# Optimization experiments

Measured on AMD Instinct MI355X. Metric: run time of the kernel, lower is better.

## Reference

```python
import jax, jax.numpy as jnp
import numpy as np

N = 8192
IN_F = 512
OUT_F = 512
ALPHA = 0.2          # LeakyReLU negative slope
NEG_INF = -9e15      # matches masked_fill value in the torch source


def setup_inputs() -> dict:
    key = jax.random.key(0)
    k1, k2, k3, k4, k5 = jax.random.split(key, 5)
    x = jax.random.normal(k1, (N, IN_F), dtype=jnp.float32)
    adj = jax.random.randint(k2, (N, N), 0, 2, dtype=jnp.int32)
    # nn.Linear(in, out, bias=False) stores weight as [out, in]
    W = jax.random.normal(k3, (OUT_F, IN_F), dtype=jnp.float32) / np.sqrt(IN_F)
    # nn.Linear(2*out, 1) weight [1, 2*out] split into the two halves that
    # act on h_i (a1) and h_j (a2): a([h_i, h_j]) = a1.h_i + a2.h_j
    a1 = jax.random.normal(k4, (OUT_F,), dtype=jnp.float32) / np.sqrt(2 * OUT_F)
    a2 = jax.random.normal(k5, (OUT_F,), dtype=jnp.float32) / np.sqrt(2 * OUT_F)
    return {"x": x, "adj": adj, "W": W, "a1": a1, "a2": a2}


def reference(x, adj, W, a1, a2):
    # h = W(x)                                  [N, OUT_F]
    h = x @ W.T
    # e[i, j] = leakyrelu(a . [h_i, h_j]) = leakyrelu(a1.h_i + a2.h_j)
    # (identical math to the N^2 concat in the source, without materializing it)
    src = h @ a1                                # [N]
    dst = h @ a2                                # [N]
    e = jax.nn.leaky_relu(src[:, None] + dst[None, :], negative_slope=ALPHA)
    e = jnp.where(adj == 0, jnp.float32(NEG_INF), e)
    attention = jax.nn.softmax(e, axis=1)       # [N, N]
    # dropout prob is 0.0 (eval-equivalent), so it is the identity
    h_prime = attention @ h                     # [N, OUT_F]
    return h_prime
```

## Files before the change

kernel.cpp:

```cpp
#include <hip/hip_runtime.h>
#include <hip/hip_bf16.h>
#include <stdint.h>

#define NN 8192
#define KF 512
#define ALPHA 0.2f
#define NT 64

typedef __bf16 bf16;
typedef __bf16 bf16x4 __attribute__((ext_vector_type(4)));
typedef __bf16 bf16x8 __attribute__((ext_vector_type(8)));
typedef float  f32x4  __attribute__((ext_vector_type(4)));
typedef float  f32x16 __attribute__((ext_vector_type(16)));

static constexpr size_t OFF_HQ  = 0;
static constexpr size_t OFF_XB  = (size_t)8 << 20;
static constexpr size_t OFF_WB  = (size_t)16 << 20;
static constexpr size_t OFF_SRC = OFF_WB + ((size_t)512 << 10);
static constexpr size_t OFF_DST = OFF_SRC + (size_t)NN * 4;
static constexpr size_t OFF_PRT = (size_t)17 << 20;
static constexpr size_t OFF_PDN = OFF_PRT + ((size_t)32 << 20);


__global__ void k_cvt(const float* __restrict__ x, const float* __restrict__ W,
                      bf16* __restrict__ xb, bf16* __restrict__ wb) {
    const int XQ = (NN * KF) / 4;
    const int TQ = XQ + (KF * KF) / 4;
    for (int i = blockIdx.x * blockDim.x + threadIdx.x; i < TQ;
         i += gridDim.x * blockDim.x) {
        const float4* s;
        bf16* d;
        int o;
        if (i < XQ) { s = (const float4*)x; d = xb; o = i; }
        else        { s = (const float4*)W; d = wb; o = i - XQ; }
        float4 v = s[o];
        bf16x4 b;
        b[0] = (bf16)v.x; b[1] = (bf16)v.y; b[2] = (bf16)v.z; b[3] = (bf16)v.w;
        *(bf16x4*)(d + (size_t)o * 4) = b;
    }
}

__global__ __launch_bounds__(256) void k_gemm(
    const bf16* __restrict__ xb, const bf16* __restrict__ wb,
    bf16* __restrict__ hQ, float* __restrict__ srcv, float* __restrict__ dstv,
    const float* __restrict__ a1, const float* __restrict__ a2) {
    const int tid = threadIdx.x;
    const int wv = tid >> 6;
    const int l = tid & 63;
    const int task = blockIdx.x * 4 + wv;
    const int rg = task >> 3, cc = task & 7;
    const int i0 = rg * 16, c0 = cc * 64;
    const int lr16 = l & 15, lk = l >> 4;

    f32x4 acc0 = {0.f,0.f,0.f,0.f}, acc1 = acc0, acc2 = acc0, acc3 = acc0;

    const bf16* ap  = xb + (size_t)(i0 + lr16) * KF + lk * 8;
    const bf16* bp0 = wb + (size_t)(c0 +  0 + lr16) * KF + lk * 8;
    const bf16* bp1 = wb + (size_t)(c0 + 16 + lr16) * KF + lk * 8;
    const bf16* bp2 = wb + (size_t)(c0 + 32 + lr16) * KF + lk * 8;
    const bf16* bp3 = wb + (size_t)(c0 + 48 + lr16) * KF + lk * 8;

#pragma unroll 4
    for (int k = 0; k < 16; ++k) {
        bf16x8 a  = *(const bf16x8*)(ap  + k * 32);
        bf16x8 b0 = *(const bf16x8*)(bp0 + k * 32);
        bf16x8 b1 = *(const bf16x8*)(bp1 + k * 32);
        bf16x8 b2 = *(const bf16x8*)(bp2 + k * 32);
        bf16x8 b3 = *(const bf16x8*)(bp3 + k * 32);
        acc0 = __builtin_amdgcn_mfma_f32_16x16x32_bf16(a, b0, acc0, 0, 0, 0);
        acc1 = __builtin_amdgcn_mfma_f32_16x16x32_bf16(a, b1, acc1, 0, 0, 0);
        acc2 = __builtin_amdgcn_mfma_f32_16x16x32_bf16(a, b2, acc2, 0, 0, 0);
        acc3 = __builtin_amdgcn_mfma_f32_16x16x32_bf16(a, b3, acc3, 0, 0, 0);
    }

    const int ib = i0 + lk * 4;
    const int jt = ib >> 6, kq = (ib >> 3) & 7, jr0 = ib & 7;
    float sr[4] = {0.f,0.f,0.f,0.f}, dr[4] = {0.f,0.f,0.f,0.f};
#pragma unroll
    for (int ct = 0; ct < 4; ++ct) {
        const f32x4 av = (ct == 0) ? acc0 : (ct == 1) ? acc1 : (ct == 2) ? acc2 : acc3;
        const int c = c0 + ct * 16 + lr16;
        const float A1 = a1[c], A2 = a2[c];
        bf16x4 hb;
#pragma unroll
        for (int r = 0; r < 4; ++r) {
            float h = av[r];
            sr[r] += h * A1;
            dr[r] += h * A2;
            hb[r] = (bf16)h;
        }
        *(bf16x4*)(hQ + ((size_t)(jt * 8 + kq) * 512 + c) * 8 + jr0) = hb;
    }
#pragma unroll
    for (int r = 0; r < 4; ++r) {
        float s = sr[r], d = dr[r];
        s += __shfl_xor(s, 1, 64); d += __shfl_xor(d, 1, 64);
        s += __shfl_xor(s, 2, 64); d += __shfl_xor(d, 2, 64);
        s += __shfl_xor(s, 4, 64); d += __shfl_xor(d, 4, 64);
        s += __shfl_xor(s, 8, 64); d += __shfl_xor(d, 8, 64);
        if (lr16 == 0) {
            atomicAdd(srcv + ib + r, s);
            atomicAdd(dstv + ib + r, d);
        }
    }
}

__global__ __launch_bounds__(512, 2) void k_attn(
    const int* __restrict__ adj, const bf16* __restrict__ hQ,
    const float* __restrict__ srcv, const float* __restrict__ dstv,
    float* __restrict__ part, float* __restrict__ pden) {
    __shared__ bf16 pl[64][72];
    __shared__ float dls[64];

    const int tid = threadIdx.x;
    const int l = tid & 63;
    const int wv = tid >> 6;
    const int bid = blockIdx.x;
    const int xg = bid & 7, qg = bid >> 3;
    const int js = xg >> 2;
    const int rt = qg * 4 + (xg & 3);
    const int i0 = rt * 64;
    const int jbase = js * 4096;

    const int pr = tid >> 3;
    const int pj = (tid & 7) * 8;
    const float si = srcv[i0 + pr];

    if (tid < 64) dls[tid] = 0.f;
    __syncthreads();

    const int lhi = l >> 5;
    const int l31 = l & 31;
    const int cA = wv * 64 + l31;

    const int*   adjp = adj  + (size_t)(i0 + pr) * NN + jbase + pj;
    const float* dstp = dstv + jbase + pj;
    const bf16*  hqb  = hQ + (size_t)cA * 8;
    const size_t tq0  = (size_t)js * 512;

    f32x16 acc00 = {0.f}, acc01 = {0.f}, acc10 = {0.f}, acc11 = {0.f};

    int4   adjA0 = *(const int4*)(adjp);
    int4   adjA1 = *(const int4*)(adjp + 4);
    float4 dstA0 = *(const float4*)(dstp);
    float4 dstA1 = *(const float4*)(dstp + 4);
    bf16x8 bfA[8], bfB[8];
#pragma unroll
    for (int k2 = 0; k2 < 4; ++k2) {
        bfA[k2 * 2]     = *(const bf16x8*)(hqb + (tq0 + k2 * 2 + lhi) * 4096);
        bfA[k2 * 2 + 1] = *(const bf16x8*)(hqb + (tq0 + k2 * 2 + lhi) * 4096 + 256);
    }
    int4 adjB0, adjB1;
    float4 dstB0, dstB1;

#define BODY(T, BFC, BFN, AJC0, AJC1, AJN0, AJN1, DSC0, DSC1, DSN0, DSN1)          \
    {                                                                              \
        const int t_ = (T);                                                        \
        if (t_ < NT - 1) {   \
            AJN0 = *(const int4*)(adjp + (t_ + 1) * 64);                           \
            AJN1 = *(const int4*)(adjp + (t_ + 1) * 64 + 4);                       \
        }                                                                          \
        {                                                                          \
            float w0,w1,w2,w3,w4,w5,w6,w7, e;                                      \
            e = si + DSC0.x; e = e > 0.f ? e : ALPHA * e; w0 = AJC0.x ? __expf(e) : 0.f; \
            e = si + DSC0.y; e = e > 0.f ? e : ALPHA * e; w1 = AJC0.y ? __expf(e) : 0.f; \
            e = si + DSC0.z; e = e > 0.f ? e : ALPHA * e; w2 = AJC0.z ? __expf(e) : 0.f; \
            e = si + DSC0.w; e = e > 0.f ? e : ALPHA * e; w3 = AJC0.w ? __expf(e) : 0.f; \
            e = si + DSC1.x; e = e > 0.f ? e : ALPHA * e; w4 = AJC1.x ? __expf(e) : 0.f; \
            e = si + DSC1.y; e = e > 0.f ? e : ALPHA * e; w5 = AJC1.y ? __expf(e) : 0.f; \
            e = si + DSC1.z; e = e > 0.f ? e : ALPHA * e; w6 = AJC1.z ? __expf(e) : 0.f; \
            e = si + DSC1.w; e = e > 0.f ? e : ALPHA * e; w7 = AJC1.w ? __expf(e) : 0.f; \
            bf16x8 pb;                                                             \
            pb[0]=(bf16)w0; pb[1]=(bf16)w1; pb[2]=(bf16)w2; pb[3]=(bf16)w3;        \
            pb[4]=(bf16)w4; pb[5]=(bf16)w5; pb[6]=(bf16)w6; pb[7]=(bf16)w7;        \
            *(bf16x8*)(&pl[pr][pj]) = pb;                                          \
            float dsum = w0+w1+w2+w3+w4+w5+w6+w7;                                  \
            dsum += __shfl_xor(dsum, 1, 64);                                       \
            dsum += __shfl_xor(dsum, 2, 64);                                       \
            dsum += __shfl_xor(dsum, 4, 64);                                       \
            if ((tid & 7) == 0) dls[pr] += dsum;                                   \
        }                                                                          \
        asm volatile("s_waitcnt lgkmcnt(0)" ::: "memory");                         \
        __builtin_amdgcn_s_barrier();                                              \
        if (t_ < NT - 1) {       \
            const size_t tqn = tq0 + (size_t)(t_ + 1) * 8;                         \
            _Pragma("unroll")                                                      \
            for (int k2 = 0; k2 < 4; ++k2) {                                       \
                BFN[k2 * 2]     = *(const bf16x8*)(hqb + (tqn + k2 * 2 + lhi) * 4096);       \
                BFN[k2 * 2 + 1] = *(const bf16x8*)(hqb + (tqn + k2 * 2 + lhi) * 4096 + 256); \
            }                                                                      \
            DSN0 = *(const float4*)(dstp + (t_ + 1) * 64);                         \
            DSN1 = *(const float4*)(dstp + (t_ + 1) * 64 + 4);                     \
        }                                                                          \
        _Pragma("unroll")                                                          \
        for (int k = 0; k < 4; ++k) {                                              \
            const int ko = k * 16 + lhi * 8;                                       \
            bf16x8 a0  = *(const bf16x8*)(&pl[l31][ko]);                           \
            bf16x8 a1f = *(const bf16x8*)(&pl[32 + l31][ko]);                      \
            acc00 = __builtin_amdgcn_mfma_f32_32x32x16_bf16(a0,  BFC[k*2],   acc00, 0,0,0); \
            acc01 = __builtin_amdgcn_mfma_f32_32x32x16_bf16(a0,  BFC[k*2+1], acc01, 0,0,0); \
            acc10 = __builtin_amdgcn_mfma_f32_32x32x16_bf16(a1f, BFC[k*2],   acc10, 0,0,0); \
            acc11 = __builtin_amdgcn_mfma_f32_32x32x16_bf16(a1f, BFC[k*2+1], acc11, 0,0,0); \
        }                                                                          \
        asm volatile("s_waitcnt lgkmcnt(0)" ::: "memory");                         \
        __builtin_amdgcn_s_barrier();                                              \
    }

    for (int tt = 0; tt < NT / 2; ++tt) {
        BODY(2 * tt,     bfA, bfB, adjA0, adjA1, adjB0, adjB1, dstA0, dstA1, dstB0, dstB1)
        BODY(2 * tt + 1, bfB, bfA, adjB0, adjB1, adjA0, adjA1, dstB0, dstB1, dstA0, dstA1)
    }
#undef BODY

    float* pp = part + (size_t)js * NN * KF;
#pragma unroll
    for (int g = 0; g < 16; ++g) {
        const int row = (g & 3) + 8 * (g >> 2) + 4 * lhi;
        pp[(size_t)(i0 + row) * KF + cA]           = acc00[g];
        pp[(size_t)(i0 + row) * KF + cA + 32]      = acc01[g];
        pp[(size_t)(i0 + 32 + row) * KF + cA]      = acc10[g];
        pp[(size_t)(i0 + 32 + row) * KF + cA + 32] = acc11[g];
    }
    if (tid < 64) pden[(size_t)js * NN + i0 + tid] = dls[tid];
}

__global__ void k_red(const float* __restrict__ part, const float* __restrict__ pden,
                      float* __restrict__ out) {
    int idx = blockIdx.x * blockDim.x + threadIdx.x;
    const float4 p0 = *(const float4*)(part + (size_t)idx * 4);
    const float4 p1 = *(const float4*)(part + (size_t)NN * KF + (size_t)idx * 4);
    int i = idx >> 7;
    float inv = 1.f / (pden[i] + pden[NN + i]);
    float4 o;
    o.x = (p0.x + p1.x) * inv;
    o.y = (p0.y + p1.y) * inv;
    o.z = (p0.z + p1.z) * inv;
    o.w = (p0.w + p1.w) * inv;
    *(float4*)(out + (size_t)idx * 4) = o;
}

extern "C" void kernel_launch(void* const* d_in, const int* in_sizes, int n_in,
                              void* d_out, int out_size, void* d_ws, size_t ws_size,
                              hipStream_t stream) {
    (void)in_sizes; (void)n_in; (void)out_size; (void)ws_size;
    const float* x  = (const float*)d_in[0];
    const int* adj  = (const int*)d_in[1];
    const float* W  = (const float*)d_in[2];
    const float* a1 = (const float*)d_in[3];
    const float* a2 = (const float*)d_in[4];
    float* out = (float*)d_out;
    char* ws = (char*)d_ws;

    bf16* hQ  = (bf16*)(ws + OFF_HQ);
    bf16* xb  = (bf16*)(ws + OFF_XB);
    bf16* wb  = (bf16*)(ws + OFF_WB);
    float* sv = (float*)(ws + OFF_SRC);
    float* dv = (float*)(ws + OFF_DST);
    float* part = (float*)(ws + OFF_PRT);
    float* pden = (float*)(ws + OFF_PDN);

    hipMemsetAsync(sv, 0, (size_t)2 * NN * sizeof(float), stream);
    k_cvt<<<2048, 256, 0, stream>>>(x, W, xb, wb);
    k_gemm<<<1024, 256, 0, stream>>>(xb, wb, hQ, sv, dv, a1, a2);
    k_attn<<<256, 512, 0, stream>>>(adj, hQ, sv, dv, part, pden);
    k_red<<<4096, 256, 0, stream>>>(part, pden, out);
}
```

Measured before the change: 507.2 us.

## Double-buffer attention LDS tile to drop one barrier per step

Double-buffers the shared P tile so each iteration needs a single barrier instead of two. The per-row denominator is kept in a register and reduced once at the end rather than updated in LDS every step. The loop is rolled back from the manual two-step unrolled macro, and next-tile prefetches are issued before the barrier. The launch-bounds occupancy hint of 2 is removed, which may raise register use and lower occupancy.

```diff
diff --git a/kernel.cpp b/kernel.cpp
--- a/kernel.cpp
+++ b/kernel.cpp
@@ -5,7 +5,7 @@
 #define NN 8192
 #define KF 512
 #define ALPHA 0.2f
-#define NT 64
+#define NTT 64
 
 typedef __bf16 bf16;
 typedef __bf16 bf16x4 __attribute__((ext_vector_type(4)));
@@ -105,12 +105,11 @@
     }
 }
 
-__global__ __launch_bounds__(512, 2) void k_attn(
+__global__ __launch_bounds__(512) void k_attn(
     const int* __restrict__ adj, const bf16* __restrict__ hQ,
     const float* __restrict__ srcv, const float* __restrict__ dstv,
     float* __restrict__ part, float* __restrict__ pden) {
-    __shared__ bf16 pl[64][72];
-    __shared__ float dls[64];
+    __shared__ bf16 pl[2][64][72];
 
     const int tid = threadIdx.x;
     const int l = tid & 63;
@@ -126,9 +125,6 @@
     const int pj = (tid & 7) * 8;
     const float si = srcv[i0 + pr];
 
-    if (tid < 64) dls[tid] = 0.f;
-    __syncthreads();
-
     const int lhi = l >> 5;
     const int l31 = l & 31;
     const int cA = wv * 64 + l31;
@@ -139,78 +135,68 @@
     const size_t tq0  = (size_t)js * 512;
 
     f32x16 acc00 = {0.f}, acc01 = {0.f}, acc10 = {0.f}, acc11 = {0.f};
-
-    int4   adjA0 = *(const int4*)(adjp);
-    int4   adjA1 = *(const int4*)(adjp + 4);
-    float4 dstA0 = *(const float4*)(dstp);
-    float4 dstA1 = *(const float4*)(dstp + 4);
-    bf16x8 bfA[8], bfB[8];
+    float dacc = 0.f;
+
+    int4   aC0 = *(const int4*)(adjp);
+    int4   aC1 = *(const int4*)(adjp + 4);
+    float4 dC0 = *(const float4*)(dstp);
+    float4 dC1 = *(const float4*)(dstp + 4);
+    bf16x8 bf[8];
 #pragma unroll
     for (int k2 = 0; k2 < 4; ++k2) {
-        bfA[k2 * 2]     = *(const bf16x8*)(hqb + (tq0 + k2 * 2 + lhi) * 4096);
-        bfA[k2 * 2 + 1] = *(const bf16x8*)(hqb + (tq0 + k2 * 2 + lhi) * 4096 + 256);
-    }
-    int4 adjB0, adjB1;
-    float4 dstB0, dstB1;
-
-#define BODY(T, BFC, BFN, AJC0, AJC1, AJN0, AJN1, DSC0, DSC1, DSN0, DSN1)          \
-    {                                                                              \
-        const int t_ = (T);                                                        \
-        if (t_ < NT - 1) {   \
-            AJN0 = *(const int4*)(adjp + (t_ + 1) * 64);                           \
-            AJN1 = *(const int4*)(adjp + (t_ + 1) * 64 + 4);                       \
-        }                                                                          \
-        {                                                                          \
-            float w0,w1,w2,w3,w4,w5,w6,w7, e;                                      \
-            e = si + DSC0.x; e = e > 0.f ? e : ALPHA * e; w0 = AJC0.x ? __expf(e) : 0.f; \
-            e = si + DSC0.y; e = e > 0.f ? e : ALPHA * e; w1 = AJC0.y ? __expf(e) : 0.f; \
-            e = si + DSC0.z; e = e > 0.f ? e : ALPHA * e; w2 = AJC0.z ? __expf(e) : 0.f; \
-            e = si + DSC0.w; e = e > 0.f ? e : ALPHA * e; w3 = AJC0.w ? __expf(e) : 0.f; \
-            e = si + DSC1.x; e = e > 0.f ? e : ALPHA * e; w4 = AJC1.x ? __expf(e) : 0.f; \
-            e = si + DSC1.y; e = e > 0.f ? e : ALPHA * e; w5 = AJC1.y ? __expf(e) : 0.f; \
-            e = si + DSC1.z; e = e > 0.f ? e : ALPHA * e; w6 = AJC1.z ? __expf(e) : 0.f; \
-            e = si + DSC1.w; e = e > 0.f ? e : ALPHA * e; w7 = AJC1.w ? __expf(e) : 0.f; \
-            bf16x8 pb;                                                             \
-            pb[0]=(bf16)w0; pb[1]=(bf16)w1; pb[2]=(bf16)w2; pb[3]=(bf16)w3;        \
-            pb[4]=(bf16)w4; pb[5]=(bf16)w5; pb[6]=(bf16)w6; pb[7]=(bf16)w7;        \
-            *(bf16x8*)(&pl[pr][pj]) = pb;                                          \
-            float dsum = w0+w1+w2+w3+w4+w5+w6+w7;                                  \
-            dsum += __shfl_xor(dsum, 1, 64);                                       \
-            dsum += __shfl_xor(dsum, 2, 64);                                       \
-            dsum += __shfl_xor(dsum, 4, 64);                                       \
-            if ((tid & 7) == 0) dls[pr] += dsum;                                   \
-        }                                                                          \
-        asm volatile("s_waitcnt lgkmcnt(0)" ::: "memory");                         \
-        __builtin_amdgcn_s_barrier();                                              \
-        if (t_ < NT - 1) {       \
-            const size_t tqn = tq0 + (size_t)(t_ + 1) * 8;                         \
-            _Pragma("unroll")                                                      \
-            for (int k2 = 0; k2 < 4; ++k2) {                                       \
-                BFN[k2 * 2]     = *(const bf16x8*)(hqb + (tqn + k2 * 2 + lhi) * 4096);       \
-                BFN[k2 * 2 + 1] = *(const bf16x8*)(hqb + (tqn + k2 * 2 + lhi) * 4096 + 256); \
-            }                                                                      \
-            DSN0 = *(const float4*)(dstp + (t_ + 1) * 64);                         \
-            DSN1 = *(const float4*)(dstp + (t_ + 1) * 64 + 4);                     \
-        }                                                                          \
-        _Pragma("unroll")                                                          \
-        for (int k = 0; k < 4; ++k) {                                              \
-            const int ko = k * 16 + lhi * 8;                                       \
-            bf16x8 a0  = *(const bf16x8*)(&pl[l31][ko]);                           \
-            bf16x8 a1f = *(const bf16x8*)(&pl[32 + l31][ko]);                      \
-            acc00 = __builtin_amdgcn_mfma_f32_32x32x16_bf16(a0,  BFC[k*2],   acc00, 0,0,0); \
-            acc01 = __builtin_amdgcn_mfma_f32_32x32x16_bf16(a0,  BFC[k*2+1], acc01, 0,0,0); \
-            acc10 = __builtin_amdgcn_mfma_f32_32x32x16_bf16(a1f, BFC[k*2],   acc10, 0,0,0); \
-            acc11 = __builtin_amdgcn_mfma_f32_32x32x16_bf16(a1f, BFC[k*2+1], acc11, 0,0,0); \
-        }                                                                          \
-        asm volatile("s_waitcnt lgkmcnt(0)" ::: "memory");                         \
-        __builtin_amdgcn_s_barrier();                                              \
-    }
-
-    for (int tt = 0; tt < NT / 2; ++tt) {
-        BODY(2 * tt,     bfA, bfB, adjA0, adjA1, adjB0, adjB1, dstA0, dstA1, dstB0, dstB1)
-        BODY(2 * tt + 1, bfB, bfA, adjB0, adjB1, adjA0, adjA1, dstB0, dstB1, dstA0, dstA1)
-    }
-#undef BODY
+        bf[k2 * 2]     = *(const bf16x8*)(hqb + (tq0 + k2 * 2 + lhi) * 4096);
+        bf[k2 * 2 + 1] = *(const bf16x8*)(hqb + (tq0 + k2 * 2 + lhi) * 4096 + 256);
+    }
+
+    for (int t = 0; t < NTT; ++t) {
+        float w0, w1, w2, w3, w4, w5, w6, w7, e;
+        e = si + dC0.x; e = fmaxf(e, ALPHA * e); w0 = aC0.x ? __expf(e) : 0.f;
+        e = si + dC0.y; e = fmaxf(e, ALPHA * e); w1 = aC0.y ? __expf(e) : 0.f;
+        e = si + dC0.z; e = fmaxf(e, ALPHA * e); w2 = aC0.z ? __expf(e) : 0.f;
+        e = si + dC0.w; e = fmaxf(e, ALPHA * e); w3 = aC0.w ? __expf(e) : 0.f;
+        e = si + dC1.x; e = fmaxf(e, ALPHA * e); w4 = aC1.x ? __expf(e) : 0.f;
+        e = si + dC1.y; e = fmaxf(e, ALPHA * e); w5 = aC1.y ? __expf(e) : 0.f;
+        e = si + dC1.z; e = fmaxf(e, ALPHA * e); w6 = aC1.z ? __expf(e) : 0.f;
+        e = si + dC1.w; e = fmaxf(e, ALPHA * e); w7 = aC1.w ? __expf(e) : 0.f;
+        bf16x8 pb;
+        pb[0] = (bf16)w0; pb[1] = (bf16)w1; pb[2] = (bf16)w2; pb[3] = (bf16)w3;
+        pb[4] = (bf16)w4; pb[5] = (bf16)w5; pb[6] = (bf16)w6; pb[7] = (bf16)w7;
+        *(bf16x8*)(&pl[t & 1][pr][pj]) = pb;
+        dacc += ((w0 + w1) + (w2 + w3)) + ((w4 + w5) + (w6 + w7));
+
+        bf16x8 bn[8];
+        if (t + 1 < NTT) {
+            aC0 = *(const int4*)(adjp + (t + 1) * 64);
+            aC1 = *(const int4*)(adjp + (t + 1) * 64 + 4);
+            dC0 = *(const float4*)(dstp + (t + 1) * 64);
+            dC1 = *(const float4*)(dstp + (t + 1) * 64 + 4);
+            const size_t tqn = tq0 + (size_t)(t + 1) * 8;
+#pragma unroll
+            for (int k2 = 0; k2 < 4; ++k2) {
+                bn[k2 * 2]     = *(const bf16x8*)(hqb + (tqn + k2 * 2 + lhi) * 4096);
+                bn[k2 * 2 + 1] = *(const bf16x8*)(hqb + (tqn + k2 * 2 + lhi) * 4096 + 256);
+            }
+        }
+
+        asm volatile("s_waitcnt lgkmcnt(0)" ::: "memory");
+        __builtin_amdgcn_s_barrier();
+
+        const bf16* plc = &pl[t & 1][0][0];
+#pragma unroll
+        for (int k = 0; k < 4; ++k) {
+            const int ko = k * 16 + lhi * 8;
+            bf16x8 a0  = *(const bf16x8*)(plc + l31 * 72 + ko);
+            bf16x8 a1f = *(const bf16x8*)(plc + (32 + l31) * 72 + ko);
+            acc00 = __builtin_amdgcn_mfma_f32_32x32x16_bf16(a0,  bf[k*2],   acc00, 0,0,0);
+            acc01 = __builtin_amdgcn_mfma_f32_32x32x16_bf16(a0,  bf[k*2+1], acc01, 0,0,0);
+            acc10 = __builtin_amdgcn_mfma_f32_32x32x16_bf16(a1f, bf[k*2],   acc10, 0,0,0);
+            acc11 = __builtin_amdgcn_mfma_f32_32x32x16_bf16(a1f, bf[k*2+1], acc11, 0,0,0);
+        }
+        if (t + 1 < NTT) {
+#pragma unroll
+            for (int q = 0; q < 8; ++q) bf[q] = bn[q];
+        }
+    }
 
     float* pp = part + (size_t)js * NN * KF;
 #pragma unroll
@@ -221,7 +207,10 @@
         pp[(size_t)(i0 + 32 + row) * KF + cA]      = acc10[g];
         pp[(size_t)(i0 + 32 + row) * KF + cA + 32] = acc11[g];
     }
-    if (tid < 64) pden[(size_t)js * NN + i0 + tid] = dls[tid];
+    dacc += __shfl_xor(dacc, 1, 64);
+    dacc += __shfl_xor(dacc, 2, 64);
+    dacc += __shfl_xor(dacc, 4, 64);
+    if ((tid & 7) == 0) pden[(size_t)js * NN + i0 + pr] = dacc;
 }
 
 __global__ void k_red(const float* __restrict__ part, const float* __restrict__ pden,
```

Result: faster. 472.3 us (-6.9%).
